# Kernel optimization log

Hardware: AMD Instinct MI355X
Metric: run time of the kernel (lower is better)

## Reference

```python
import jax, jax.numpy as jnp
import numpy as np

TEMP = 0.5  # init temperature
EPS = 1e-12  # F.normalize eps


def setup_inputs() -> dict:
    key = jax.random.key(0)
    k1, k2 = jax.random.split(key)
    batch_embedding = jax.random.normal(k1, (4096, 256), dtype=jnp.float32)
    labels = jax.random.randint(k2, (4096,), 0, 512, dtype=jnp.int64)
    return {"batch_embedding": batch_embedding, "labels": labels}


def reference(batch_embedding, labels):
    n = labels.shape[0]
    dt = batch_embedding.dtype
    # row-normalize; cosine_similarity of normalized rows == norm @ norm.T
    nrm = jnp.linalg.norm(batch_embedding, axis=1, keepdims=True)
    norm = batch_embedding / jnp.maximum(nrm, EPS)
    sim = norm @ norm.T  # [n, n]
    mask = (labels[:, None] == labels[None, :]).astype(dt)  # same-label pairs (incl. diagonal)
    eye = jnp.eye(n, dtype=dt)
    exp_sim = jnp.exp(sim / TEMP) * (1.0 - eye)  # zero diagonal
    pos = mask * exp_sim
    neg_sum = jnp.sum(exp_sim - pos, axis=1)  # per-row negative sum
    ratio = pos / (pos + neg_sum[:, None])
    loss_mat = -jnp.log((1.0 - mask) + ratio + eye)
    nnz = jnp.count_nonzero(loss_mat).astype(dt)
    return jnp.sum(loss_mat) / nnz
```

## Files before the change

### kernel.cpp

```cpp
#include <hip/hip_runtime.h>
#include <hip/hip_bf16.h>


#define N_ROWS 4096
#define K_DIM  256

typedef __attribute__((ext_vector_type(4))) float float4v;
typedef __attribute__((ext_vector_type(4))) float f4;
typedef __attribute__((ext_vector_type(4))) int   int4v;
typedef __attribute__((ext_vector_type(2))) long  long2v;

#define PK_OFF    0
#define PART_OFF  (2 * 1024 * 1024)
#define ACC_OFF   (PART_OFF + 4 * 64 * N_ROWS * 4)

__device__ __forceinline__ void gll16(const void* g, void* l) {
    __builtin_amdgcn_global_load_lds(
        (const __attribute__((address_space(1))) unsigned int*)g,
        (__attribute__((address_space(3))) unsigned int*)l, 16, 0, 0);
}

__global__ void normalize_kernel(const float* __restrict__ emb,
                                 unsigned char* __restrict__ pk8,
                                 float* __restrict__ acc) {
    int tile = blockIdx.x, t = threadIdx.x;
    __shared__ float lds[16 * 256];
    __shared__ float sc[16];
    const f4* src = (const f4*)(emb + tile * 16 * 256);
    f4* dst4 = (f4*)lds;
    #pragma unroll
    for (int it = 0; it < 4; ++it) dst4[t + 256 * it] = src[t + 256 * it];
    __syncthreads();
    int wave = t >> 6, lane = t & 63;
    int row = wave * 4 + (lane >> 4);
    float s = 0.f;
    #pragma unroll
    for (int m = 0; m < 16; ++m) {
        float x = lds[row * 256 + (lane & 15) + 16 * m];
        s += x * x;
    }
    s += __shfl_xor(s, 1); s += __shfl_xor(s, 2);
    s += __shfl_xor(s, 4); s += __shfl_xor(s, 8);
    float scale = 1.0f / fmaxf(sqrtf(s), 1e-12f);
    if ((lane & 15) == 0) sc[row] = scale;
    __syncthreads();
    int u = t >> 6, quad = (t >> 4) & 3, r16 = t & 15;
    float s8 = sc[r16] * 8.0f;
    const float* lr = lds + r16 * 256;
    int4v wv;
    #pragma unroll
    for (int wi = 0; wi < 4; ++wi) {
        int h  = wi >> 1;
        int j0 = (wi & 1) * 4;
        int kb = quad * 8 + (2 * u + h) * 32 + j0;
        float v0 = lr[kb + 0] * s8, v1 = lr[kb + 1] * s8;
        float v2 = lr[kb + 2] * s8, v3 = lr[kb + 3] * s8;
        int wd = __builtin_amdgcn_cvt_pk_fp8_f32(v0, v1, 0, 0);
        wd     = __builtin_amdgcn_cvt_pk_fp8_f32(v2, v3, wd, 1);
        wv[wi] = wd;
    }
    *(int4v*)(pk8 + tile * 4096 + t * 16) = wv;
    if (tile == 0 && t < 4) acc[t] = 0.0f;
}

__global__ __launch_bounds__(256, 2)
void negsum_kernel(const unsigned char* __restrict__ pk8,
                   const int* __restrict__ labels,
                   float* __restrict__ part) {
    __shared__ __align__(16) unsigned char As8[32768];
    __shared__ __align__(16) unsigned char Bs8[32768];
    int t = threadIdx.x;
    int w = t >> 6, lane = t & 63;
    int lane16 = lane & 15, quad = lane >> 4;
    int bi = blockIdx.x >> 5, bj = blockIdx.x & 31;
    int wi = w >> 1, wj = w & 1;

    int ibase = bi * 128 + wi * 64;
    int jbase = bj * 128 + wj * 64;
    int labi[16], labj[4];
    #pragma unroll
    for (int it = 0; it < 4; ++it)
        #pragma unroll
        for (int r = 0; r < 4; ++r)
            labi[it * 4 + r] = labels[ibase + it * 16 + quad * 4 + r];
    #pragma unroll
    for (int jt = 0; jt < 4; ++jt)
        labj[jt] = labels[jbase + jt * 16 + lane16];

    const char* pkb = (const char*)pk8;

    {
        int isA   = (w < 2);
        int wloc  = isA ? w : (w - 2);
        int btile = isA ? bi : bj;
        unsigned char* panel = isA ? As8 : Bs8;
        #pragma unroll
        for (int u = 0; u < 16; ++u) {
            int tl = wloc * 4 + (u >> 2), cs = u & 3;
            gll16(pkb + (((btile * 8 + tl) << 12) | (cs << 10)) + lane * 16,
                  panel + (((tl << 2) | cs) << 10));
        }
    }

    float4v acc[4][4];
    #pragma unroll
    for (int a = 0; a < 4; ++a)
        #pragma unroll
        for (int b = 0; b < 4; ++b)
            acc[a][b] = (float4v){0.f, 0.f, 0.f, 0.f};

    __syncthreads();

    #pragma unroll
    for (int cs = 0; cs < 4; ++cs) {
        long2v av[4], bv[4];
        #pragma unroll
        for (int it = 0; it < 4; ++it)
            av[it] = *(const long2v*)(As8 + (((((wi * 4 + it) << 2) | cs) << 10)) + lane * 16);
        #pragma unroll
        for (int jt = 0; jt < 4; ++jt)
            bv[jt] = *(const long2v*)(Bs8 + (((((wj * 4 + jt) << 2) | cs) << 10)) + lane * 16);
        #pragma unroll
        for (int h = 0; h < 2; ++h)
            #pragma unroll
            for (int it = 0; it < 4; ++it)
                #pragma unroll
                for (int jt = 0; jt < 4; ++jt)
                    acc[it][jt] = __builtin_amdgcn_mfma_f32_16x16x32_fp8_fp8(
                        av[it][h], bv[jt][h], acc[it][jt], 0, 0, 0);
    }

    float ex[4] = {0,0,0,0}, pe[4] = {0,0,0,0};
    float tt[4] = {0,0,0,0}, pc[4] = {0,0,0,0};
    #pragma unroll
    for (int it = 0; it < 4; ++it) {
        #pragma unroll
        for (int jt = 0; jt < 4; ++jt) {
            int j = jbase + jt * 16 + lane16;
            #pragma unroll
            for (int r = 0; r < 4; ++r) {
                int i = ibase + it * 16 + quad * 4 + r;
                float t2 = acc[it][jt][r] * 0.03125f;
                float e  = __expf(t2);
                bool keep = (i != j);
                bool same = (labi[it * 4 + r] == labj[jt]);
                ex[jt] += keep ? e : 0.0f;
                float m = (same && keep) ? 1.0f : 0.0f;
                pe[jt] = fmaf(m, e,  pe[jt]);
                tt[jt] = fmaf(m, t2, tt[jt]);
                pc[jt] += m;
            }
        }
    }
    int i64 = bi * 2 + wi;
    #pragma unroll
    for (int jt = 0; jt < 4; ++jt) {
        float v0 = ex[jt], v1 = pe[jt], v2 = tt[jt], v3 = pc[jt];
        v0 += __shfl_xor(v0, 16); v0 += __shfl_xor(v0, 32);
        v1 += __shfl_xor(v1, 16); v1 += __shfl_xor(v1, 32);
        v2 += __shfl_xor(v2, 16); v2 += __shfl_xor(v2, 32);
        v3 += __shfl_xor(v3, 16); v3 += __shfl_xor(v3, 32);
        if (quad == 0) {
            int col = jbase + jt * 16 + lane16;
            part[((0 * 64 + i64) << 12) + col] = v0;
            part[((1 * 64 + i64) << 12) + col] = v1;
            part[((2 * 64 + i64) << 12) + col] = v2;
            part[((3 * 64 + i64) << 12) + col] = v3;
        }
    }
}

__global__ void rowreduce_kernel(const float* __restrict__ part,
                                 float* __restrict__ acc,
                                 float* __restrict__ out) {
    int j = blockIdx.x * 256 + threadIdx.x;
    float ex = 0.f, pe = 0.f, tt = 0.f, pc = 0.f;
    for (int ch = 0; ch < 64; ++ch) {
        ex += part[((0 * 64 + ch) << 12) + j];
        pe += part[((1 * 64 + ch) << 12) + j];
        tt += part[((2 * 64 + ch) << 12) + j];
        pc += part[((3 * 64 + ch) << 12) + j];
    }
    float lsum = 0.f;
    if (pc > 0.f) {
        float n = ex - pe;
        lsum = pc * logf(n) + pe / n - tt;
    } else {
        pc = 0.f;
    }
    #pragma unroll
    for (int off = 32; off > 0; off >>= 1) {
        lsum += __shfl_down(lsum, off, 64);
        pc   += __shfl_down(pc,   off, 64);
    }
    __shared__ float sl[4], sc2[4];
    int wave = threadIdx.x >> 6, lane = threadIdx.x & 63;
    if (lane == 0) { sl[wave] = lsum; sc2[wave] = pc; }
    __syncthreads();
    if (threadIdx.x == 0) {
        atomicAdd(&acc[0], sl[0] + sl[1] + sl[2] + sl[3]);
        atomicAdd(&acc[1], sc2[0] + sc2[1] + sc2[2] + sc2[3]);
        __threadfence();
        int ticket = atomicAdd((int*)(acc + 2), 1);
        if (ticket == 15) {
            float ls = atomicAdd(&acc[0], 0.0f);
            float cs = atomicAdd(&acc[1], 0.0f);
            out[0] = ls / cs;
        }
    }
}

extern "C" void kernel_launch(void* const* d_in, const int* in_sizes, int n_in,
                              void* d_out, int out_size, void* d_ws, size_t ws_size,
                              hipStream_t stream) {
    const float* emb    = (const float*)d_in[0];
    const int*   labels = (const int*)d_in[1];
    float* out = (float*)d_out;
    char*  ws  = (char*)d_ws;

    unsigned char* pk8  = (unsigned char*)(ws + PK_OFF);
    float*         part = (float*)(ws + PART_OFF);
    float*         acc  = (float*)(ws + ACC_OFF);

    normalize_kernel<<<N_ROWS / 16, 256, 0, stream>>>(emb, pk8, acc);
    negsum_kernel<<<1024, 256, 0, stream>>>(pk8, labels, part);
    rowreduce_kernel<<<16, 256, 0, stream>>>(part, acc, out);
}
```

Baseline: 81.50 us.

## Fuse three kernels into one persistent kernel with grid barriers

Merges the normalize, pairwise-similarity, and row-reduce kernels into a single persistent kernel of 512 blocks. Software grid barriers on atomic counters separate the phases, and each block handles two GEMM tiles. Control counters are cleared with a memset. This removes two kernel-launch gaps and the tail effects between them. In exchange it requires all 512 blocks to be co-resident, which holds at 2 blocks per CU on 256 CUs and otherwise deadlocks. It also adds barrier spin cost, and the one-tile-at-a-time loop has no overlap between loads and compute.

```diff
diff --git a/kernel.cpp b/kernel.cpp
--- a/kernel.cpp
+++ b/kernel.cpp
@@ -4,6 +4,7 @@
 
 #define N_ROWS 4096
 #define K_DIM  256
+#define GRID   512
 
 typedef __attribute__((ext_vector_type(4))) float float4v;
 typedef __attribute__((ext_vector_type(4))) float f4;
@@ -12,7 +13,7 @@
 
 #define PK_OFF    0
 #define PART_OFF  (2 * 1024 * 1024)
-#define ACC_OFF   (PART_OFF + 4 * 64 * N_ROWS * 4)
+#define CTRL_OFF  (PART_OFF + 4 * 64 * N_ROWS * 4)
 
 __device__ __forceinline__ void gll16(const void* g, void* l) {
     __builtin_amdgcn_global_load_lds(
@@ -20,192 +21,228 @@
         (__attribute__((address_space(3))) unsigned int*)l, 16, 0, 0);
 }
 
-__global__ void normalize_kernel(const float* __restrict__ emb,
-                                 unsigned char* __restrict__ pk8,
-                                 float* __restrict__ acc) {
-    int tile = blockIdx.x, t = threadIdx.x;
-    __shared__ float lds[16 * 256];
-    __shared__ float sc[16];
-    const f4* src = (const f4*)(emb + tile * 16 * 256);
-    f4* dst4 = (f4*)lds;
-    #pragma unroll
-    for (int it = 0; it < 4; ++it) dst4[t + 256 * it] = src[t + 256 * it];
+__device__ __forceinline__ void gridbar(int* c) {
     __syncthreads();
-    int wave = t >> 6, lane = t & 63;
-    int row = wave * 4 + (lane >> 4);
-    float s = 0.f;
-    #pragma unroll
-    for (int m = 0; m < 16; ++m) {
-        float x = lds[row * 256 + (lane & 15) + 16 * m];
-        s += x * x;
-    }
-    s += __shfl_xor(s, 1); s += __shfl_xor(s, 2);
-    s += __shfl_xor(s, 4); s += __shfl_xor(s, 8);
-    float scale = 1.0f / fmaxf(sqrtf(s), 1e-12f);
-    if ((lane & 15) == 0) sc[row] = scale;
+    if (threadIdx.x == 0) {
+        __threadfence();
+        __hip_atomic_fetch_add(c, 1, __ATOMIC_ACQ_REL, __HIP_MEMORY_SCOPE_AGENT);
+        while (__hip_atomic_load(c, __ATOMIC_ACQUIRE, __HIP_MEMORY_SCOPE_AGENT) < GRID)
+            __builtin_amdgcn_s_sleep(2);
+        __threadfence();
+    }
     __syncthreads();
-    int u = t >> 6, quad = (t >> 4) & 3, r16 = t & 15;
-    float s8 = sc[r16] * 8.0f;
-    const float* lr = lds + r16 * 256;
-    int4v wv;
-    #pragma unroll
-    for (int wi = 0; wi < 4; ++wi) {
-        int h  = wi >> 1;
-        int j0 = (wi & 1) * 4;
-        int kb = quad * 8 + (2 * u + h) * 32 + j0;
-        float v0 = lr[kb + 0] * s8, v1 = lr[kb + 1] * s8;
-        float v2 = lr[kb + 2] * s8, v3 = lr[kb + 3] * s8;
-        int wd = __builtin_amdgcn_cvt_pk_fp8_f32(v0, v1, 0, 0);
-        wd     = __builtin_amdgcn_cvt_pk_fp8_f32(v2, v3, wd, 1);
-        wv[wi] = wd;
-    }
-    *(int4v*)(pk8 + tile * 4096 + t * 16) = wv;
-    if (tile == 0 && t < 4) acc[t] = 0.0f;
 }
 
 __global__ __launch_bounds__(256, 2)
-void negsum_kernel(const unsigned char* __restrict__ pk8,
-                   const int* __restrict__ labels,
-                   float* __restrict__ part) {
-    __shared__ __align__(16) unsigned char As8[32768];
-    __shared__ __align__(16) unsigned char Bs8[32768];
+void fused_kernel(const float* __restrict__ emb,
+                  const int* __restrict__ labels,
+                  unsigned char* __restrict__ pk8,
+                  float* __restrict__ part,
+                  float* __restrict__ ctrl,
+                  float* __restrict__ out) {
+    __shared__ __align__(16) unsigned char smem[65536];
     int t = threadIdx.x;
     int w = t >> 6, lane = t & 63;
-    int lane16 = lane & 15, quad = lane >> 4;
-    int bi = blockIdx.x >> 5, bj = blockIdx.x & 31;
-    int wi = w >> 1, wj = w & 1;
-
-    int ibase = bi * 128 + wi * 64;
-    int jbase = bj * 128 + wj * 64;
-    int labi[16], labj[4];
-    #pragma unroll
-    for (int it = 0; it < 4; ++it)
-        #pragma unroll
-        for (int r = 0; r < 4; ++r)
-            labi[it * 4 + r] = labels[ibase + it * 16 + quad * 4 + r];
-    #pragma unroll
-    for (int jt = 0; jt < 4; ++jt)
-        labj[jt] = labels[jbase + jt * 16 + lane16];
-
-    const char* pkb = (const char*)pk8;
+    int* ctrli = (int*)ctrl;
+
+    if (blockIdx.x < 256) {
+        int tile = blockIdx.x;
+        float* lds = (float*)smem;
+        float* sc  = (float*)(smem + 16384);
+        const f4* src = (const f4*)(emb + tile * 16 * 256);
+        f4* dst4 = (f4*)lds;
+        #pragma unroll
+        for (int it = 0; it < 4; ++it) dst4[t + 256 * it] = src[t + 256 * it];
+        __syncthreads();
+        int row = w * 4 + (lane >> 4);
+        float s = 0.f;
+        #pragma unroll
+        for (int m = 0; m < 16; ++m) {
+            float x = lds[row * 256 + (lane & 15) + 16 * m];
+            s += x * x;
+        }
+        s += __shfl_xor(s, 1); s += __shfl_xor(s, 2);
+        s += __shfl_xor(s, 4); s += __shfl_xor(s, 8);
+        float scale = 1.0f / fmaxf(sqrtf(s), 1e-12f);
+        if ((lane & 15) == 0) sc[row] = scale;
+        __syncthreads();
+        int u = t >> 6, quad = (t >> 4) & 3, r16 = t & 15;
+        float s8 = sc[r16] * 8.0f;
+        const float* lr = lds + r16 * 256;
+        int4v wv;
+        #pragma unroll
+        for (int wi = 0; wi < 4; ++wi) {
+            int h  = wi >> 1;
+            int j0 = (wi & 1) * 4;
+            int kb = quad * 8 + (2 * u + h) * 32 + j0;
+            float v0 = lr[kb + 0] * s8, v1 = lr[kb + 1] * s8;
+            float v2 = lr[kb + 2] * s8, v3 = lr[kb + 3] * s8;
+            int wd = __builtin_amdgcn_cvt_pk_fp8_f32(v0, v1, 0, 0);
+            wd     = __builtin_amdgcn_cvt_pk_fp8_f32(v2, v3, wd, 1);
+            wv[wi] = wd;
+        }
+        *(int4v*)(pk8 + tile * 4096 + t * 16) = wv;
+    }
+
+    gridbar(ctrli + 2);
 
     {
-        int isA   = (w < 2);
-        int wloc  = isA ? w : (w - 2);
-        int btile = isA ? bi : bj;
-        unsigned char* panel = isA ? As8 : Bs8;
-        #pragma unroll
-        for (int u = 0; u < 16; ++u) {
-            int tl = wloc * 4 + (u >> 2), cs = u & 3;
-            gll16(pkb + (((btile * 8 + tl) << 12) | (cs << 10)) + lane * 16,
-                  panel + (((tl << 2) | cs) << 10));
-        }
-    }
-
-    float4v acc[4][4];
-    #pragma unroll
-    for (int a = 0; a < 4; ++a)
-        #pragma unroll
-        for (int b = 0; b < 4; ++b)
-            acc[a][b] = (float4v){0.f, 0.f, 0.f, 0.f};
-
-    __syncthreads();
-
-    #pragma unroll
-    for (int cs = 0; cs < 4; ++cs) {
-        long2v av[4], bv[4];
-        #pragma unroll
-        for (int it = 0; it < 4; ++it)
-            av[it] = *(const long2v*)(As8 + (((((wi * 4 + it) << 2) | cs) << 10)) + lane * 16);
-        #pragma unroll
-        for (int jt = 0; jt < 4; ++jt)
-            bv[jt] = *(const long2v*)(Bs8 + (((((wj * 4 + jt) << 2) | cs) << 10)) + lane * 16);
-        #pragma unroll
-        for (int h = 0; h < 2; ++h)
+        unsigned char* As8 = smem;
+        unsigned char* Bs8 = smem + 32768;
+        int lane16 = lane & 15, quad = lane >> 4;
+        int wi = w >> 1, wj = w & 1;
+        const char* pkb = (const char*)pk8;
+
+        for (int it2 = 0; it2 < 2; ++it2) {
+            int bt = blockIdx.x + it2 * GRID;
+            int bi = bt >> 5, bj = bt & 31;
+            int ibase = bi * 128 + wi * 64;
+            int jbase = bj * 128 + wj * 64;
+            int labi[16], labj[4];
             #pragma unroll
             for (int it = 0; it < 4; ++it)
                 #pragma unroll
+                for (int r = 0; r < 4; ++r)
+                    labi[it * 4 + r] = labels[ibase + it * 16 + quad * 4 + r];
+            #pragma unroll
+            for (int jt = 0; jt < 4; ++jt)
+                labj[jt] = labels[jbase + jt * 16 + lane16];
+
+            __syncthreads();
+            {
+                int isA   = (w < 2);
+                int wloc  = isA ? w : (w - 2);
+                int btile = isA ? bi : bj;
+                unsigned char* panel = isA ? As8 : Bs8;
+                #pragma unroll
+                for (int u = 0; u < 16; ++u) {
+                    int tl = wloc * 4 + (u >> 2), cs = u & 3;
+                    gll16(pkb + (((btile * 8 + tl) << 12) | (cs << 10)) + lane * 16,
+                          panel + (((tl << 2) | cs) << 10));
+                }
+            }
+
+            float4v acc[4][4];
+            #pragma unroll
+            for (int a = 0; a < 4; ++a)
+                #pragma unroll
+                for (int b = 0; b < 4; ++b)
+                    acc[a][b] = (float4v){0.f, 0.f, 0.f, 0.f};
+
+            __syncthreads();
+
+            #pragma unroll
+            for (int cs = 0; cs < 4; ++cs) {
+                long2v av[4], bv[4];
+                #pragma unroll
+                for (int it = 0; it < 4; ++it)
+                    av[it] = *(const long2v*)(As8 + (((((wi * 4 + it) << 2) | cs) << 10)) + lane * 16);
+                #pragma unroll
                 for (int jt = 0; jt < 4; ++jt)
-                    acc[it][jt] = __builtin_amdgcn_mfma_f32_16x16x32_fp8_fp8(
-                        av[it][h], bv[jt][h], acc[it][jt], 0, 0, 0);
-    }
-
-    float ex[4] = {0,0,0,0}, pe[4] = {0,0,0,0};
-    float tt[4] = {0,0,0,0}, pc[4] = {0,0,0,0};
-    #pragma unroll
-    for (int it = 0; it < 4; ++it) {
-        #pragma unroll
-        for (int jt = 0; jt < 4; ++jt) {
-            int j = jbase + jt * 16 + lane16;
-            #pragma unroll
-            for (int r = 0; r < 4; ++r) {
-                int i = ibase + it * 16 + quad * 4 + r;
-                float t2 = acc[it][jt][r] * 0.03125f;
-                float e  = __expf(t2);
-                bool keep = (i != j);
-                bool same = (labi[it * 4 + r] == labj[jt]);
-                ex[jt] += keep ? e : 0.0f;
-                float m = (same && keep) ? 1.0f : 0.0f;
-                pe[jt] = fmaf(m, e,  pe[jt]);
-                tt[jt] = fmaf(m, t2, tt[jt]);
-                pc[jt] += m;
-            }
-        }
-    }
-    int i64 = bi * 2 + wi;
-    #pragma unroll
-    for (int jt = 0; jt < 4; ++jt) {
-        float v0 = ex[jt], v1 = pe[jt], v2 = tt[jt], v3 = pc[jt];
-        v0 += __shfl_xor(v0, 16); v0 += __shfl_xor(v0, 32);
-        v1 += __shfl_xor(v1, 16); v1 += __shfl_xor(v1, 32);
-        v2 += __shfl_xor(v2, 16); v2 += __shfl_xor(v2, 32);
-        v3 += __shfl_xor(v3, 16); v3 += __shfl_xor(v3, 32);
-        if (quad == 0) {
-            int col = jbase + jt * 16 + lane16;
-            part[((0 * 64 + i64) << 12) + col] = v0;
-            part[((1 * 64 + i64) << 12) + col] = v1;
-            part[((2 * 64 + i64) << 12) + col] = v2;
-            part[((3 * 64 + i64) << 12) + col] = v3;
-        }
-    }
-}
-
-__global__ void rowreduce_kernel(const float* __restrict__ part,
-                                 float* __restrict__ acc,
-                                 float* __restrict__ out) {
-    int j = blockIdx.x * 256 + threadIdx.x;
-    float ex = 0.f, pe = 0.f, tt = 0.f, pc = 0.f;
-    for (int ch = 0; ch < 64; ++ch) {
-        ex += part[((0 * 64 + ch) << 12) + j];
-        pe += part[((1 * 64 + ch) << 12) + j];
-        tt += part[((2 * 64 + ch) << 12) + j];
-        pc += part[((3 * 64 + ch) << 12) + j];
-    }
-    float lsum = 0.f;
-    if (pc > 0.f) {
-        float n = ex - pe;
-        lsum = pc * logf(n) + pe / n - tt;
-    } else {
-        pc = 0.f;
-    }
-    #pragma unroll
-    for (int off = 32; off > 0; off >>= 1) {
-        lsum += __shfl_down(lsum, off, 64);
-        pc   += __shfl_down(pc,   off, 64);
-    }
-    __shared__ float sl[4], sc2[4];
-    int wave = threadIdx.x >> 6, lane = threadIdx.x & 63;
-    if (lane == 0) { sl[wave] = lsum; sc2[wave] = pc; }
-    __syncthreads();
-    if (threadIdx.x == 0) {
-        atomicAdd(&acc[0], sl[0] + sl[1] + sl[2] + sl[3]);
-        atomicAdd(&acc[1], sc2[0] + sc2[1] + sc2[2] + sc2[3]);
-        __threadfence();
-        int ticket = atomicAdd((int*)(acc + 2), 1);
-        if (ticket == 15) {
-            float ls = atomicAdd(&acc[0], 0.0f);
-            float cs = atomicAdd(&acc[1], 0.0f);
-            out[0] = ls / cs;
+                    bv[jt] = *(const long2v*)(Bs8 + (((((wj * 4 + jt) << 2) | cs) << 10)) + lane * 16);
+                #pragma unroll
+                for (int h = 0; h < 2; ++h)
+                    #pragma unroll
+                    for (int it = 0; it < 4; ++it)
+                        #pragma unroll
+                        for (int jt = 0; jt < 4; ++jt)
+                            acc[it][jt] = __builtin_amdgcn_mfma_f32_16x16x32_fp8_fp8(
+                                av[it][h], bv[jt][h], acc[it][jt], 0, 0, 0);
+            }
+
+            float ex[4] = {0,0,0,0}, pe[4] = {0,0,0,0};
+            float tt[4] = {0,0,0,0}, pc[4] = {0,0,0,0};
+            #pragma unroll
+            for (int it = 0; it < 4; ++it) {
+                #pragma unroll
+                for (int jt = 0; jt < 4; ++jt) {
+                    int j = jbase + jt * 16 + lane16;
+                    #pragma unroll
+                    for (int r = 0; r < 4; ++r) {
+                        int i = ibase + it * 16 + quad * 4 + r;
+                        float t2 = acc[it][jt][r] * 0.03125f;
+                        float e  = __expf(t2);
+                        bool keep = (i != j);
+                        bool same = (labi[it * 4 + r] == labj[jt]);
+                        ex[jt] += keep ? e : 0.0f;
+                        float m = (same && keep) ? 1.0f : 0.0f;
+                        pe[jt] = fmaf(m, e,  pe[jt]);
+                        tt[jt] = fmaf(m, t2, tt[jt]);
+                        pc[jt] += m;
+                    }
+                }
+            }
+            int i64 = bi * 2 + wi;
+            #pragma unroll
+            for (int jt = 0; jt < 4; ++jt) {
+                float v0 = ex[jt], v1 = pe[jt], v2 = tt[jt], v3 = pc[jt];
+                v0 += __shfl_xor(v0, 16); v0 += __shfl_xor(v0, 32);
+                v1 += __shfl_xor(v1, 16); v1 += __shfl_xor(v1, 32);
+                v2 += __shfl_xor(v2, 16); v2 += __shfl_xor(v2, 32);
+                v3 += __shfl_xor(v3, 16); v3 += __shfl_xor(v3, 32);
+                if (quad == 0) {
+                    int col = jbase + jt * 16 + lane16;
+                    part[((0 * 64 + i64) << 12) + col] = v0;
+                    part[((1 * 64 + i64) << 12) + col] = v1;
+                    part[((2 * 64 + i64) << 12) + col] = v2;
+                    part[((3 * 64 + i64) << 12) + col] = v3;
+                }
+            }
+        }
+    }
+
+    gridbar(ctrli + 3);
+
+    {
+        int rl = t & 7;
+        int sl = t >> 3;
+        int row = blockIdx.x * 8 + rl;
+        float s[4];
+        #pragma unroll
+        for (int st = 0; st < 4; ++st) {
+            int ch0 = sl * 2;
+            s[st] = part[((st * 64 + ch0)     << 12) + row]
+                  + part[((st * 64 + ch0 + 1) << 12) + row];
+        }
+        #pragma unroll
+        for (int st = 0; st < 4; ++st) {
+            s[st] += __shfl_xor(s[st], 8);
+            s[st] += __shfl_xor(s[st], 16);
+            s[st] += __shfl_xor(s[st], 32);
+        }
+        float* red = (float*)smem;
+        if (lane < 8) {
+            #pragma unroll
+            for (int st = 0; st < 4; ++st)
+                red[(w * 4 + st) * 8 + lane] = s[st];
+        }
+        __syncthreads();
+        if (t < 8) {
+            float ex = red[0*8+t] + red[4*8+t] + red[8*8+t]  + red[12*8+t];
+            float pe = red[1*8+t] + red[5*8+t] + red[9*8+t]  + red[13*8+t];
+            float tt = red[2*8+t] + red[6*8+t] + red[10*8+t] + red[14*8+t];
+            float pc = red[3*8+t] + red[7*8+t] + red[11*8+t] + red[15*8+t];
+            float lsum = 0.f;
+            if (pc > 0.f) {
+                float n = ex - pe;
+                lsum = pc * logf(n) + pe / n - tt;
+            } else {
+                pc = 0.f;
+            }
+            lsum += __shfl_xor(lsum, 1); pc += __shfl_xor(pc, 1);
+            lsum += __shfl_xor(lsum, 2); pc += __shfl_xor(pc, 2);
+            lsum += __shfl_xor(lsum, 4); pc += __shfl_xor(pc, 4);
+            if (t == 0) {
+                atomicAdd(&ctrl[0], lsum);
+                atomicAdd(&ctrl[1], pc);
+                __threadfence();
+                int ticket = atomicAdd(ctrli + 4, 1);
+                if (ticket == GRID - 1) {
+                    float ls = atomicAdd(&ctrl[0], 0.0f);
+                    float cs = atomicAdd(&ctrl[1], 0.0f);
+                    out[0] = ls / cs;
+                }
+            }
         }
     }
 }
@@ -220,9 +257,8 @@
 
     unsigned char* pk8  = (unsigned char*)(ws + PK_OFF);
     float*         part = (float*)(ws + PART_OFF);
-    float*         acc  = (float*)(ws + ACC_OFF);
-
-    normalize_kernel<<<N_ROWS / 16, 256, 0, stream>>>(emb, pk8, acc);
-    negsum_kernel<<<1024, 256, 0, stream>>>(pk8, labels, part);
-    rowreduce_kernel<<<16, 256, 0, stream>>>(part, acc, out);
-}
+    float*         ctrl = (float*)(ws + CTRL_OFF);
+
+    hipMemsetAsync(ctrl, 0, 32, stream);
+    fused_kernel<<<GRID, 256, 0, stream>>>(emb, labels, pk8, part, ctrl, out);
+}
```

Measured after the change: 195.0 us. 139% more time.

## Load A operands to registers, remap blocks per XCD, widen row reduction

Applied to the files above, without the earlier changes.

The negsum kernel no longer stages the A panel in LDS. Each wave loads its A fragments straight from global memory into registers, which halves LDS use and allows three blocks per CU. Block indices are remapped so each XCD handles a contiguous group of row tiles, meant to improve L2 reuse of the A data. The row-reduce kernel now runs 128 blocks, with 8 threads per row splitting the 64 partial chunks, to increase parallelism, at the cost of more atomics.

```diff
diff --git a/kernel.cpp b/kernel.cpp
--- a/kernel.cpp
+++ b/kernel.cpp
@@ -63,20 +63,37 @@
     if (tile == 0 && t < 4) acc[t] = 0.0f;
 }
 
-__global__ __launch_bounds__(256, 2)
+__global__ __launch_bounds__(256, 3)
 void negsum_kernel(const unsigned char* __restrict__ pk8,
                    const int* __restrict__ labels,
                    float* __restrict__ part) {
-    __shared__ __align__(16) unsigned char As8[32768];
     __shared__ __align__(16) unsigned char Bs8[32768];
     int t = threadIdx.x;
     int w = t >> 6, lane = t & 63;
     int lane16 = lane & 15, quad = lane >> 4;
-    int bi = blockIdx.x >> 5, bj = blockIdx.x & 31;
+    int xcd = blockIdx.x & 7, local = blockIdx.x >> 3;
+    int bi = xcd * 4 + (local >> 5);
+    int bj = local & 31;
     int wi = w >> 1, wj = w & 1;
 
     int ibase = bi * 128 + wi * 64;
     int jbase = bj * 128 + wj * 64;
+    const char* pkb = (const char*)pk8;
+
+    #pragma unroll
+    for (int u = 0; u < 8; ++u) {
+        int c8 = w * 8 + u, tl = c8 >> 2, cs = c8 & 3;
+        gll16(pkb + (((bj * 8 + tl) << 12) | (cs << 10)) + lane * 16,
+              Bs8 + (c8 << 10));
+    }
+    long2v av[4][4];
+    #pragma unroll
+    for (int it = 0; it < 4; ++it)
+        #pragma unroll
+        for (int cs = 0; cs < 4; ++cs)
+            av[it][cs] = *(const long2v*)(pkb
+                + (((bi * 8 + wi * 4 + it) << 12) | (cs << 10)) + lane * 16);
+
     int labi[16], labj[4];
     #pragma unroll
     for (int it = 0; it < 4; ++it)
@@ -87,21 +104,6 @@
     for (int jt = 0; jt < 4; ++jt)
         labj[jt] = labels[jbase + jt * 16 + lane16];
 
-    const char* pkb = (const char*)pk8;
-
-    {
-        int isA   = (w < 2);
-        int wloc  = isA ? w : (w - 2);
-        int btile = isA ? bi : bj;
-        unsigned char* panel = isA ? As8 : Bs8;
-        #pragma unroll
-        for (int u = 0; u < 16; ++u) {
-            int tl = wloc * 4 + (u >> 2), cs = u & 3;
-            gll16(pkb + (((btile * 8 + tl) << 12) | (cs << 10)) + lane * 16,
-                  panel + (((tl << 2) | cs) << 10));
-        }
-    }
-
     float4v acc[4][4];
     #pragma unroll
     for (int a = 0; a < 4; ++a)
@@ -113,13 +115,11 @@
 
     #pragma unroll
     for (int cs = 0; cs < 4; ++cs) {
-        long2v av[4], bv[4];
-        #pragma unroll
-        for (int it = 0; it < 4; ++it)
-            av[it] = *(const long2v*)(As8 + (((((wi * 4 + it) << 2) | cs) << 10)) + lane * 16);
+        long2v bv[4];
         #pragma unroll
         for (int jt = 0; jt < 4; ++jt)
-            bv[jt] = *(const long2v*)(Bs8 + (((((wj * 4 + jt) << 2) | cs) << 10)) + lane * 16);
+            bv[jt] = *(const long2v*)(Bs8
+                     + (((((wj * 4 + jt) << 2) | cs) << 10)) + lane * 16);
         #pragma unroll
         for (int h = 0; h < 2; ++h)
             #pragma unroll
@@ -127,7 +127,7 @@
                 #pragma unroll
                 for (int jt = 0; jt < 4; ++jt)
                     acc[it][jt] = __builtin_amdgcn_mfma_f32_16x16x32_fp8_fp8(
-                        av[it][h], bv[jt][h], acc[it][jt], 0, 0, 0);
+                        av[it][cs][h], bv[jt][h], acc[it][jt], 0, 0, 0);
     }
 
     float ex[4] = {0,0,0,0}, pe[4] = {0,0,0,0};
@@ -173,36 +173,45 @@
 __global__ void rowreduce_kernel(const float* __restrict__ part,
                                  float* __restrict__ acc,
                                  float* __restrict__ out) {
-    int j = blockIdx.x * 256 + threadIdx.x;
-    float ex = 0.f, pe = 0.f, tt = 0.f, pc = 0.f;
-    for (int ch = 0; ch < 64; ++ch) {
-        ex += part[((0 * 64 + ch) << 12) + j];
-        pe += part[((1 * 64 + ch) << 12) + j];
-        tt += part[((2 * 64 + ch) << 12) + j];
-        pc += part[((3 * 64 + ch) << 12) + j];
-    }
-    float lsum = 0.f;
-    if (pc > 0.f) {
-        float n = ex - pe;
-        lsum = pc * logf(n) + pe / n - tt;
-    } else {
-        pc = 0.f;
-    }
-    #pragma unroll
-    for (int off = 32; off > 0; off >>= 1) {
-        lsum += __shfl_down(lsum, off, 64);
-        pc   += __shfl_down(pc,   off, 64);
-    }
-    __shared__ float sl[4], sc2[4];
-    int wave = threadIdx.x >> 6, lane = threadIdx.x & 63;
-    if (lane == 0) { sl[wave] = lsum; sc2[wave] = pc; }
-    __syncthreads();
-    if (threadIdx.x == 0) {
-        atomicAdd(&acc[0], sl[0] + sl[1] + sl[2] + sl[3]);
-        atomicAdd(&acc[1], sc2[0] + sc2[1] + sc2[2] + sc2[3]);
+    int t = threadIdx.x;
+    int rl = t >> 3, sl = t & 7;
+    int row = blockIdx.x * 32 + rl;
+    float s[4];
+    #pragma unroll
+    for (int st = 0; st < 4; ++st) {
+        float v = 0.f;
+        #pragma unroll
+        for (int c = 0; c < 8; ++c)
+            v += part[((st * 64 + (sl * 8 + c)) << 12) + row];
+        s[st] = v;
+    }
+    #pragma unroll
+    for (int st = 0; st < 4; ++st) {
+        s[st] += __shfl_xor(s[st], 1);
+        s[st] += __shfl_xor(s[st], 2);
+        s[st] += __shfl_xor(s[st], 4);
+    }
+    float lsum = 0.f, pcm = 0.f;
+    if (sl == 0 && s[3] > 0.f) {
+        float n = s[0] - s[1];
+        lsum = s[3] * logf(n) + s[1] / n - s[2];
+        pcm  = s[3];
+    }
+    #pragma unroll
+    for (int m = 1; m < 64; m <<= 1) {
+        lsum += __shfl_xor(lsum, m);
+        pcm  += __shfl_xor(pcm,  m);
+    }
+    __shared__ float sl4[4], sc4[4];
+    int wave = t >> 6, lane = t & 63;
+    if (lane == 0) { sl4[wave] = lsum; sc4[wave] = pcm; }
+    __syncthreads();
+    if (t == 0) {
+        atomicAdd(&acc[0], sl4[0] + sl4[1] + sl4[2] + sl4[3]);
+        atomicAdd(&acc[1], sc4[0] + sc4[1] + sc4[2] + sc4[3]);
         __threadfence();
         int ticket = atomicAdd((int*)(acc + 2), 1);
-        if (ticket == 15) {
+        if (ticket == 127) {
             float ls = atomicAdd(&acc[0], 0.0f);
             float cs = atomicAdd(&acc[1], 0.0f);
             out[0] = ls / cs;
@@ -224,5 +233,5 @@
 
     normalize_kernel<<<N_ROWS / 16, 256, 0, stream>>>(emb, pk8, acc);
     negsum_kernel<<<1024, 256, 0, stream>>>(pk8, labels, part);
-    rowreduce_kernel<<<16, 256, 0, stream>>>(part, acc, out);
-}
+    rowreduce_kernel<<<128, 256, 0, stream>>>(part, acc, out);
+}
```

Result: faster. 78.91 us, median of 2 (-3.2%).
